# Performance work log

Measured on AMD Instinct MI355X. Metric: run time of the kernel, lower is better.

## Reference

```python
import jax, jax.numpy as jnp
import numpy as np

EPS = 1e-5
CH = 8            # channels_per_head
HID = 4           # max(CH // reduction, 4)
SCALE = CH ** -0.5


def _layernorm(x, g, b):
    mu = jnp.mean(x, axis=-1, keepdims=True)
    var = jnp.mean(jnp.square(x - mu), axis=-1, keepdims=True)
    return (x - mu) * jax.lax.rsqrt(var + EPS) * g + b


def setup_inputs() -> dict:
    key = jax.random.key(0)
    ks = jax.random.split(key, 12)
    s = 1.0 / np.sqrt(CH)
    sh = 1.0 / np.sqrt(HID)
    return {
        "x": jax.random.normal(ks[0], (32, 4, CH, 256, 256), dtype=jnp.float32),
        "Wq": jax.random.uniform(ks[1], (CH, CH), jnp.float32, -s, s),
        "Wk": jax.random.uniform(ks[2], (CH, CH), jnp.float32, -s, s),
        "Wv": jax.random.uniform(ks[3], (CH, CH), jnp.float32, -s, s),
        "Wo": jax.random.uniform(ks[4], (CH, CH), jnp.float32, -s, s),
        "bo": jax.random.uniform(ks[5], (CH,), jnp.float32, -s, s),
        "W1": jax.random.uniform(ks[6], (HID, CH), jnp.float32, -s, s),
        "b1": jax.random.uniform(ks[7], (HID,), jnp.float32, -s, s),
        "W2": jax.random.uniform(ks[8], (CH, HID), jnp.float32, -sh, sh),
        "b2": jax.random.uniform(ks[9], (CH,), jnp.float32, -sh, sh),
        "g1": jnp.ones((CH,), jnp.float32),
        "beta1": jnp.zeros((CH,), jnp.float32),
        "g2": jnp.ones((CH,), jnp.float32),
        "beta2": jnp.zeros((CH,), jnp.float32),
        "gate": jnp.full((1,), 0.5, jnp.float32),
    }


def reference(x, Wq, Wk, Wv, Wo, bo, W1, b1, W2, b2, g1, beta1, g2, beta2, gate):
    # x: (B, n_heads, CH, H, W); pool over spatial dims -> (B, n_heads, CH)
    x_pooled = jnp.mean(x, axis=(-2, -1))
    xn = _layernorm(x_pooled, g1, beta1)
    Q = xn @ Wq.T
    K = xn @ Wk.T
    V = xn @ Wv.T
    # tiny attention across heads: scores (B, n_heads, n_heads)
    attn = jax.nn.softmax(jnp.einsum('bhc,bgc->bhg', Q, K) * SCALE, axis=-1)
    attn_out = jnp.einsum('bhg,bgc->bhc', attn, V) @ Wo.T + bo
    x_attn = x_pooled + attn_out
    xn2 = _layernorm(x_attn, g2, beta2)
    ffn = jax.nn.gelu(xn2 @ W1.T + b1, approximate=False) @ W2.T + b2
    x_out = x_attn + ffn
    g = jax.nn.sigmoid(gate)
    aw = g * (x_out - x_pooled) + x_pooled      # (B, n_heads, CH)
    return x * (1.0 + aw[..., None, None])
```

## Files before the change

kernel.cpp:

```cpp
#include <hip/hip_runtime.h>
#include <math.h>

#define CH 8
#define NH 4
#define HID 4
#define SPATIAL 65536
#define NSLICE 1024
#define EPS 1e-5f

typedef float nf4 __attribute__((ext_vector_type(4)));

__global__ void pool_kernel(const float* __restrict__ x, float* __restrict__ pooled) {
    const int slice = blockIdx.x;
    const nf4* xs = (const nf4*)(x + (size_t)slice * SPATIAL);
    float sum = 0.f;
    for (int k = threadIdx.x; k < SPATIAL / 4; k += blockDim.x) {
        nf4 v = xs[k];
        sum += (v.x + v.y) + (v.z + v.w);
    }
    for (int off = 32; off; off >>= 1) sum += __shfl_down(sum, off, 64);
    __shared__ float part[4];
    const int lane = threadIdx.x & 63, wv = threadIdx.x >> 6;
    if (lane == 0) part[wv] = sum;
    __syncthreads();
    if (threadIdx.x == 0) {
        float s = (part[0] + part[1]) + (part[2] + part[3]);
        pooled[slice] = s * (1.0f / SPATIAL);
    }
}

__global__ __launch_bounds__(256, 4)
void scale_fused(const float* __restrict__ x,
                 const float* __restrict__ pooled,
                 const float* __restrict__ Wq, const float* __restrict__ Wk,
                 const float* __restrict__ Wv, const float* __restrict__ Wo,
                 const float* __restrict__ bo,
                 const float* __restrict__ W1, const float* __restrict__ b1,
                 const float* __restrict__ W2, const float* __restrict__ b2,
                 const float* __restrict__ g1, const float* __restrict__ beta1,
                 const float* __restrict__ g2, const float* __restrict__ beta2,
                 const float* __restrict__ gate,
                 float* __restrict__ out) {
    const int blk   = blockIdx.x;
    const int slice = blk >> 1;
    const int half  = blk & 1;
    const int b     = slice >> 5;
    const int hh    = (slice >> 3) & 3;
    const int cc    = slice & 7;
    const int tid   = threadIdx.x;

    __shared__ float Kl[NH][CH], Vl[NH][CH], fac[NH][CH];

    float xp[CH], Q[CH];
    if (tid < NH) {
        const float* pr = pooled + b * (NH * CH) + tid * CH;
#pragma unroll
        for (int c = 0; c < CH; ++c) xp[c] = pr[c];
        float mu = 0.f;
#pragma unroll
        for (int c = 0; c < CH; ++c) mu += xp[c];
        mu *= 0.125f;
        float var = 0.f;
#pragma unroll
        for (int c = 0; c < CH; ++c) { float d = xp[c] - mu; var += d * d; }
        var *= 0.125f;
        float rs = rsqrtf(var + EPS);
        float xn[CH];
#pragma unroll
        for (int c = 0; c < CH; ++c) xn[c] = (xp[c] - mu) * rs * g1[c] + beta1[c];
#pragma unroll
        for (int c = 0; c < CH; ++c) {
            float q = 0.f, k = 0.f, v = 0.f;
#pragma unroll
            for (int j = 0; j < CH; ++j) {
                q += xn[j] * Wq[c * CH + j];
                k += xn[j] * Wk[c * CH + j];
                v += xn[j] * Wv[c * CH + j];
            }
            Q[c] = q; Kl[tid][c] = k; Vl[tid][c] = v;
        }
    }
    __syncthreads();
    if (tid < NH) {
        float sc[NH], mx = -1e30f;
#pragma unroll
        for (int g = 0; g < NH; ++g) {
            float s = 0.f;
#pragma unroll
            for (int c = 0; c < CH; ++c) s += Q[c] * Kl[g][c];
            s *= 0.35355339059327373f;
            sc[g] = s; mx = fmaxf(mx, s);
        }
        float den = 0.f;
#pragma unroll
        for (int g = 0; g < NH; ++g) { sc[g] = __expf(sc[g] - mx); den += sc[g]; }
        const float inv = 1.0f / den;
        float ao[CH];
#pragma unroll
        for (int c = 0; c < CH; ++c) {
            float a = 0.f;
#pragma unroll
            for (int g = 0; g < NH; ++g) a += sc[g] * Vl[g][c];
            ao[c] = a * inv;
        }
        float xa[CH];
#pragma unroll
        for (int c = 0; c < CH; ++c) {
            float o = bo[c];
#pragma unroll
            for (int j = 0; j < CH; ++j) o += ao[j] * Wo[c * CH + j];
            xa[c] = xp[c] + o;
        }
        float mu = 0.f;
#pragma unroll
        for (int c = 0; c < CH; ++c) mu += xa[c];
        mu *= 0.125f;
        float var = 0.f;
#pragma unroll
        for (int c = 0; c < CH; ++c) { float d = xa[c] - mu; var += d * d; }
        var *= 0.125f;
        float rs = rsqrtf(var + EPS);
        float xn2[CH];
#pragma unroll
        for (int c = 0; c < CH; ++c) xn2[c] = (xa[c] - mu) * rs * g2[c] + beta2[c];
        float h1[HID];
#pragma unroll
        for (int i = 0; i < HID; ++i) {
            float t = b1[i];
#pragma unroll
            for (int c = 0; c < CH; ++c) t += xn2[c] * W1[i * CH + c];
            h1[i] = 0.5f * t * (1.0f + erff(t * 0.70710678118654752f));
        }
        const float gs = 1.0f / (1.0f + __expf(-gate[0]));
#pragma unroll
        for (int c = 0; c < CH; ++c) {
            float f = b2[c];
#pragma unroll
            for (int i = 0; i < HID; ++i) f += h1[i] * W2[c * HID + i];
            float xo = xa[c] + f;
            fac[tid][c] = 1.0f + gs * (xo - xp[c]) + xp[c];
        }
    }
    __syncthreads();
    const float f = fac[hh][cc];

    const nf4* xs = (const nf4*)x   + (size_t)slice * (SPATIAL / 4) + (size_t)half * 8192;
    nf4*       os = (nf4*)out       + (size_t)slice * (SPATIAL / 4) + (size_t)half * 8192;
    for (int k = tid; k < 8192; k += 256) {
        nf4 v = xs[k];
        v *= f;
        __builtin_nontemporal_store(v, &os[k]);
    }
}

extern "C" void kernel_launch(void* const* d_in, const int* in_sizes, int n_in,
                              void* d_out, int out_size, void* d_ws, size_t ws_size,
                              hipStream_t stream) {
    const float* x     = (const float*)d_in[0];
    const float* Wq    = (const float*)d_in[1];
    const float* Wk    = (const float*)d_in[2];
    const float* Wv    = (const float*)d_in[3];
    const float* Wo    = (const float*)d_in[4];
    const float* bo    = (const float*)d_in[5];
    const float* W1    = (const float*)d_in[6];
    const float* b1    = (const float*)d_in[7];
    const float* W2    = (const float*)d_in[8];
    const float* b2    = (const float*)d_in[9];
    const float* g1    = (const float*)d_in[10];
    const float* beta1 = (const float*)d_in[11];
    const float* g2    = (const float*)d_in[12];
    const float* beta2 = (const float*)d_in[13];
    const float* gate  = (const float*)d_in[14];
    float* out = (float*)d_out;

    float* pooled = (float*)d_ws;

    pool_kernel<<<NSLICE, 256, 0, stream>>>(x, pooled);
    scale_fused<<<NSLICE * 2, 256, 0, stream>>>(x, pooled,
                                                Wq, Wk, Wv, Wo, bo,
                                                W1, b1, W2, b2,
                                                g1, beta1, g2, beta2,
                                                gate, out);
}
```

Before: 130.2 us.

## Fuse pooling and scaling into one cooperative kernel with grid sync

```diff
diff --git a/kernel.cpp b/kernel.cpp
--- a/kernel.cpp
+++ b/kernel.cpp
@@ -1,5 +1,8 @@
 #include <hip/hip_runtime.h>
+#include <hip/hip_cooperative_groups.h>
 #include <math.h>
+
+namespace cg = cooperative_groups;
 
 #define CH 8
 #define NH 4
@@ -10,46 +13,44 @@
 
 typedef float nf4 __attribute__((ext_vector_type(4)));
 
-__global__ void pool_kernel(const float* __restrict__ x, float* __restrict__ pooled) {
-    const int slice = blockIdx.x;
-    const nf4* xs = (const nf4*)(x + (size_t)slice * SPATIAL);
-    float sum = 0.f;
-    for (int k = threadIdx.x; k < SPATIAL / 4; k += blockDim.x) {
-        nf4 v = xs[k];
-        sum += (v.x + v.y) + (v.z + v.w);
+__global__ __launch_bounds__(256, 2)
+void fused_all(const float* __restrict__ x,
+               const float* __restrict__ Wq, const float* __restrict__ Wk,
+               const float* __restrict__ Wv, const float* __restrict__ Wo,
+               const float* __restrict__ bo,
+               const float* __restrict__ W1, const float* __restrict__ b1,
+               const float* __restrict__ W2, const float* __restrict__ b2,
+               const float* __restrict__ g1, const float* __restrict__ beta1,
+               const float* __restrict__ g2, const float* __restrict__ beta2,
+               const float* __restrict__ gate,
+               float* __restrict__ out,
+               float* __restrict__ pooled) {
+    const int tid = threadIdx.x;
+    const int s0  = blockIdx.x * 2;
+    const int b   = s0 >> 5;
+
+    __shared__ float part[2][4];
+    __shared__ float Kl[NH][CH], Vl[NH][CH], fac[NH][CH];
+
+#pragma unroll
+    for (int si = 0; si < 2; ++si) {
+        const nf4* xs = (const nf4*)x + (size_t)(s0 + si) * (SPATIAL / 4);
+        float sum = 0.f;
+#pragma unroll 8
+        for (int k = tid; k < SPATIAL / 4; k += 256) {
+            nf4 v = xs[k];
+            sum += (v.x + v.y) + (v.z + v.w);
+        }
+        for (int off = 32; off; off >>= 1) sum += __shfl_down(sum, off, 64);
+        if ((tid & 63) == 0) part[si][tid >> 6] = sum;
     }
-    for (int off = 32; off; off >>= 1) sum += __shfl_down(sum, off, 64);
-    __shared__ float part[4];
-    const int lane = threadIdx.x & 63, wv = threadIdx.x >> 6;
-    if (lane == 0) part[wv] = sum;
     __syncthreads();
-    if (threadIdx.x == 0) {
-        float s = (part[0] + part[1]) + (part[2] + part[3]);
-        pooled[slice] = s * (1.0f / SPATIAL);
+    if (tid < 2) {
+        float s = (part[tid][0] + part[tid][1]) + (part[tid][2] + part[tid][3]);
+        pooled[s0 + tid] = s * (1.0f / SPATIAL);
     }
-}
 
-__global__ __launch_bounds__(256, 4)
-void scale_fused(const float* __restrict__ x,
-                 const float* __restrict__ pooled,
-                 const float* __restrict__ Wq, const float* __restrict__ Wk,
-                 const float* __restrict__ Wv, const float* __restrict__ Wo,
-                 const float* __restrict__ bo,
-                 const float* __restrict__ W1, const float* __restrict__ b1,
-                 const float* __restrict__ W2, const float* __restrict__ b2,
-                 const float* __restrict__ g1, const float* __restrict__ beta1,
-                 const float* __restrict__ g2, const float* __restrict__ beta2,
-                 const float* __restrict__ gate,
-                 float* __restrict__ out) {
-    const int blk   = blockIdx.x;
-    const int slice = blk >> 1;
-    const int half  = blk & 1;
-    const int b     = slice >> 5;
-    const int hh    = (slice >> 3) & 3;
-    const int cc    = slice & 7;
-    const int tid   = threadIdx.x;
-
-    __shared__ float Kl[NH][CH], Vl[NH][CH], fac[NH][CH];
+    cg::this_grid().sync();
 
     float xp[CH], Q[CH];
     if (tid < NH) {
@@ -142,14 +143,19 @@
         }
     }
     __syncthreads();
-    const float f = fac[hh][cc];
 
-    const nf4* xs = (const nf4*)x   + (size_t)slice * (SPATIAL / 4) + (size_t)half * 8192;
-    nf4*       os = (nf4*)out       + (size_t)slice * (SPATIAL / 4) + (size_t)half * 8192;
-    for (int k = tid; k < 8192; k += 256) {
-        nf4 v = xs[k];
-        v *= f;
-        __builtin_nontemporal_store(v, &os[k]);
+#pragma unroll
+    for (int si = 0; si < 2; ++si) {
+        const int sl = s0 + si;
+        const float f = fac[(sl >> 3) & 3][sl & 7];
+        const nf4* xs = (const nf4*)x + (size_t)sl * (SPATIAL / 4);
+        nf4*       os = (nf4*)out     + (size_t)sl * (SPATIAL / 4);
+#pragma unroll 4
+        for (int k = tid; k < SPATIAL / 4; k += 256) {
+            nf4 v = xs[k];
+            v *= f;
+            __builtin_nontemporal_store(v, &os[k]);
+        }
     }
 }
 
@@ -172,13 +178,17 @@
     const float* beta2 = (const float*)d_in[13];
     const float* gate  = (const float*)d_in[14];
     float* out = (float*)d_out;
-
     float* pooled = (float*)d_ws;
 
-    pool_kernel<<<NSLICE, 256, 0, stream>>>(x, pooled);
-    scale_fused<<<NSLICE * 2, 256, 0, stream>>>(x, pooled,
-                                                Wq, Wk, Wv, Wo, bo,
-                                                W1, b1, W2, b2,
-                                                g1, beta1, g2, beta2,
-                                                gate, out);
+    void* args[] = {
+        (void*)&x,
+        (void*)&Wq, (void*)&Wk, (void*)&Wv, (void*)&Wo, (void*)&bo,
+        (void*)&W1, (void*)&b1, (void*)&W2, (void*)&b2,
+        (void*)&g1, (void*)&beta1, (void*)&g2, (void*)&beta2,
+        (void*)&gate,
+        (void*)&out, (void*)&pooled
+    };
+    hipLaunchCooperativeKernel((const void*)fused_all,
+                               dim3(NSLICE / 2), dim3(256),
+                               args, 0, stream);
 }
```

Result: slower. 185.8 us (+42.8%).
